# Kernel optimization log

Hardware: AMD Instinct MI355X
Metric: run time of the kernel (lower is better)

Reference implementation:

```python
import jax, jax.numpy as jnp
import numpy as np

B, Nc, Ns, Nz, Nx, K = 2, 128, 2048, 256, 256, 4


def setup_inputs() -> dict:
    key = jax.random.key(0)
    k1, k2, k3 = jax.random.split(key, 3)
    # RF channel data: [B, Nc, Ns, K]
    rf = jax.random.normal(k1, (B, Nc, Ns, K), dtype=jnp.float32)
    # Imaging grid point coordinates (meters), ~4 cm field: [B, Nz, Nx, 3]
    g = jax.random.uniform(k2, (B, Nz, Nx, 3), dtype=jnp.float32) * 0.04
    # Receiver element positions (meters): [B, Nc, 3]
    pr = jax.random.uniform(k3, (B, Nc, 3), dtype=jnp.float32) * 0.04
    # Acquisition params per batch: [c0 (m/s), fs (Hz), t0 (s), unused]
    p = jnp.tile(jnp.array([1540.0, 40.0e6, 0.0, 0.0], dtype=jnp.float32), (B, 1))
    return {"rf": rf, "g": g, "pr": pr, "p": p}


def reference(rf, g, pr, p):
    # rf: [B, Nc, Ns, K]; g: [B, Nz, Nx, 3]; pr: [B, Nc, 3]; p: [B, 4]
    b, nc, ns, k = rf.shape
    nz, nx = g.shape[1], g.shape[2]
    m = nz * nx

    c0 = p[:, 0][:, None, None, None]
    fs = p[:, 1][:, None, None, None]
    t0 = p[:, 2][:, None, None, None]

    d_tx = g[..., 2]  # [B, Nz, Nx] transmit path = depth coordinate
    # receive path: distance from each receiver to each pixel -> [B, Nc, Nz, Nx]
    d_rx = jnp.linalg.norm(g[:, None, :, :, :] - pr[:, :, None, None, :], axis=-1)
    # fractional sample index of the round-trip delay
    samples = fs * (t0 + (d_rx + d_tx[:, None, :, :])) / c0  # [B, Nc, Nz, Nx]
    s = samples.reshape(b, nc, m)

    # batch_interp_regular_1d_grid with x_ref_min=0, x_ref_max=Ns-1 on Ns points
    # -> unit grid spacing, constant extension (clamp) outside the grid.
    s = jnp.clip(s, 0.0, float(ns - 1))
    i0 = jnp.clip(jnp.floor(s).astype(jnp.int32), 0, ns - 2)  # [B, Nc, M]
    w = (s - i0.astype(s.dtype))[..., None]                   # [B, Nc, M, 1]

    idx0 = jnp.broadcast_to(i0[..., None], (b, nc, m, k))
    y0 = jnp.take_along_axis(rf, idx0, axis=2)      # [B, Nc, M, K]
    y1 = jnp.take_along_axis(rf, idx0 + 1, axis=2)  # [B, Nc, M, K]
    interp = y0 * (1.0 - w) + y1 * w

    # delay-and-sum over channels, then back to image layout [B, Nz, Nx, K]
    y_das = jnp.sum(interp, axis=1).reshape(b, nz, nx, k)
    return y_das
```

## Files before the change

### kernel.cpp

```cpp
#include <hip/hip_runtime.h>


#define NBATCH 2
#define NC 128
#define NS 2048
#define NK 4
#define NM 65536

#define THREADS 1024
#define PX_PER_THREAD 4
#define PX_PER_BLOCK (THREADS * PX_PER_THREAD)
#define C_PER_BLOCK 16
#define N_CHUNKS (NC / C_PER_BLOCK)
#define N_TILES (NM / PX_PER_BLOCK)
#define NBLOCKS (NBATCH * N_TILES * N_CHUNKS)
#define SLICE_F4 (NS * NK / 4)

#define PART_BYTES ((size_t)N_CHUNKS * NBATCH * NM * NK * 4)

typedef float f32x4 __attribute__((ext_vector_type(4)));

__device__ __forceinline__ void stage_channel(const float* slice, float4* lbuf, int t) {
#pragma unroll
    for (int r = 0; r < SLICE_F4 / THREADS; ++r) {
        const int d = r * THREADS + t;
        __builtin_amdgcn_global_load_lds(
            (const __attribute__((address_space(1))) void*)(slice + (size_t)d * 4),
            (__attribute__((address_space(3))) void*)(lbuf + d),
            16, 0, 0);
    }
}

template <bool ATOMIC>
__global__ __launch_bounds__(THREADS, 8) void das_kernel(
    const float* __restrict__ rf, const float* __restrict__ g,
    const float* __restrict__ pr, const float* __restrict__ p,
    float* __restrict__ dst)
{
    __shared__ float4 sbuf[2][SLICE_F4];

    const int bid   = blockIdx.x;
    const int chunk = bid & (N_CHUNKS - 1);
    const int tile  = (bid >> 3) & (N_TILES - 1);
    const int b     = bid >> 7;
    const int t     = threadIdx.x;
    const int px0   = tile * PX_PER_BLOCK;

    const float c0v = p[b * 4 + 0];
    const float fsv = p[b * 4 + 1];
    const float t0v = p[b * 4 + 2];
    const float scale = fsv / c0v;
    const float sb0   = scale * t0v;

    float gx[PX_PER_THREAD], gy[PX_PER_THREAD], gzv[PX_PER_THREAD];
#pragma unroll
    for (int j = 0; j < PX_PER_THREAD; ++j) {
        const int m = px0 + j * THREADS + t;
        const float* gp = g + ((size_t)b * NM + m) * 3;
        gx[j]  = gp[0];
        gy[j]  = gp[1];
        gzv[j] = gp[2];
    }

    float4 acc[PX_PER_THREAD];
#pragma unroll
    for (int j = 0; j < PX_PER_THREAD; ++j) acc[j] = make_float4(0.f, 0.f, 0.f, 0.f);

    const int ch0 = chunk * C_PER_BLOCK;
    const float* slice0 = rf + (size_t)(b * NC + ch0) * NS * NK;

    stage_channel(slice0, &sbuf[0][0], t);

    for (int cc = 0; cc < C_PER_BLOCK; ++cc) {
        __syncthreads();
        if (cc + 1 < C_PER_BLOCK)
            stage_channel(slice0 + (size_t)(cc + 1) * NS * NK,
                          &sbuf[(cc + 1) & 1][0], t);

        const float4* lb = &sbuf[cc & 1][0];
        const float* prp = pr + ((size_t)(b * NC + ch0 + cc)) * 3;
        const float prx = prp[0], pry = prp[1], prz = prp[2];

#pragma unroll
        for (int j = 0; j < PX_PER_THREAD; ++j) {
            const float dx = gx[j]  - prx;
            const float dy = gy[j]  - pry;
            const float dz = gzv[j] - prz;
            const float drx = __builtin_amdgcn_sqrtf(fmaf(dx, dx, fmaf(dy, dy, dz * dz)));
            float s = fmaf(scale, gzv[j] + drx, sb0);
            s = fminf(fmaxf(s, 0.0f), (float)(NS - 1));
            const float fi = fminf(floorf(s), (float)(NS - 2));
            const float w  = s - fi;
            const float wm = 1.0f - w;
            const int i0 = (int)fi;
            const float4 y0 = lb[i0];
            const float4 y1 = lb[i0 + 1];
            acc[j].x = fmaf(y0.x, wm, fmaf(y1.x, w, acc[j].x));
            acc[j].y = fmaf(y0.y, wm, fmaf(y1.y, w, acc[j].y));
            acc[j].z = fmaf(y0.z, wm, fmaf(y1.z, w, acc[j].z));
            acc[j].w = fmaf(y0.w, wm, fmaf(y1.w, w, acc[j].w));
        }
    }

    if (ATOMIC) {
        float* ob = dst + (size_t)b * NM * NK;
#pragma unroll
        for (int j = 0; j < PX_PER_THREAD; ++j) {
            const int m = px0 + j * THREADS + t;
            float* op = ob + (size_t)m * NK;
            atomicAdd(op + 0, acc[j].x);
            atomicAdd(op + 1, acc[j].y);
            atomicAdd(op + 2, acc[j].z);
            atomicAdd(op + 3, acc[j].w);
        }
    } else {
        f32x4* pw = (f32x4*)dst + (size_t)(chunk * NBATCH + b) * NM;
#pragma unroll
        for (int j = 0; j < PX_PER_THREAD; ++j) {
            const int m = px0 + j * THREADS + t;
            const f32x4 v = {acc[j].x, acc[j].y, acc[j].z, acc[j].w};
            __builtin_nontemporal_store(v, pw + m);
        }
    }
}

__global__ __launch_bounds__(256) void reduce_kernel(
    const f32x4* __restrict__ part, f32x4* __restrict__ out)
{
    const int i = blockIdx.x * 256 + threadIdx.x;
    const size_t stride = (size_t)NBATCH * NM;
    f32x4 a = __builtin_nontemporal_load(part + i);
#pragma unroll
    for (int c = 1; c < N_CHUNKS; ++c) {
        const f32x4 v = __builtin_nontemporal_load(part + c * stride + i);
        a += v;
    }
    out[i] = a;
}

extern "C" void kernel_launch(void* const* d_in, const int* in_sizes, int n_in,
                              void* d_out, int out_size, void* d_ws, size_t ws_size,
                              hipStream_t stream) {
    (void)in_sizes; (void)n_in;
    const float* rf = (const float*)d_in[0];
    const float* g  = (const float*)d_in[1];
    const float* pr = (const float*)d_in[2];
    const float* p  = (const float*)d_in[3];
    float* out = (float*)d_out;

    if (ws_size >= PART_BYTES) {
        das_kernel<false><<<NBLOCKS, THREADS, 0, stream>>>(rf, g, pr, p, (float*)d_ws);
        reduce_kernel<<<(NBATCH * NM) / 256, 256, 0, stream>>>((const f32x4*)d_ws,
                                                               (f32x4*)out);
    } else {
        (void)hipMemsetAsync(d_out, 0, (size_t)out_size * sizeof(float), stream);
        das_kernel<true><<<NBLOCKS, THREADS, 0, stream>>>(rf, g, pr, p, out);
    }
}
```

Baseline: 92.10 us.

## Stage RF slices in LDS as fp16 via register prefetch instead of direct global-to-LDS

Each channel's RF slice is now converted to half precision and stored in LDS at half the size. Staging goes through registers: the next slice is loaded early and written to LDS after the compute loop, replacing the asynchronous global_load_lds path. The aim is to halve LDS footprint and gather bandwidth. The costs are extra convert instructions on both store and gather, fp16 rounding of the RF data, and a halved occupancy hint in launch_bounds.

Result: faster. 86.97 us, median of 3 (-5.6%).

```diff
diff --git a/kernel.cpp b/kernel.cpp
--- a/kernel.cpp
+++ b/kernel.cpp
@@ -1,4 +1,5 @@
 #include <hip/hip_runtime.h>
+#include <hip/hip_fp16.h>
 
 
 #define NBATCH 2
@@ -14,30 +15,29 @@
 #define N_CHUNKS (NC / C_PER_BLOCK)
 #define N_TILES (NM / PX_PER_BLOCK)
 #define NBLOCKS (NBATCH * N_TILES * N_CHUNKS)
-#define SLICE_F4 (NS * NK / 4)
 
 #define PART_BYTES ((size_t)N_CHUNKS * NBATCH * NM * NK * 4)
 
 typedef float f32x4 __attribute__((ext_vector_type(4)));
 
-__device__ __forceinline__ void stage_channel(const float* slice, float4* lbuf, int t) {
-#pragma unroll
-    for (int r = 0; r < SLICE_F4 / THREADS; ++r) {
-        const int d = r * THREADS + t;
-        __builtin_amdgcn_global_load_lds(
-            (const __attribute__((address_space(1))) void*)(slice + (size_t)d * 4),
-            (__attribute__((address_space(3))) void*)(lbuf + d),
-            16, 0, 0);
-    }
+__device__ __forceinline__ uint4 cvt8(float4 a, float4 b) {
+    const __half2 h0 = __floats2half2_rn(a.x, a.y);
+    const __half2 h1 = __floats2half2_rn(a.z, a.w);
+    const __half2 h2 = __floats2half2_rn(b.x, b.y);
+    const __half2 h3 = __floats2half2_rn(b.z, b.w);
+    return make_uint4(__builtin_bit_cast(unsigned, h0),
+                      __builtin_bit_cast(unsigned, h1),
+                      __builtin_bit_cast(unsigned, h2),
+                      __builtin_bit_cast(unsigned, h3));
 }
 
 template <bool ATOMIC>
-__global__ __launch_bounds__(THREADS, 8) void das_kernel(
+__global__ __launch_bounds__(THREADS, 4) void das_kernel(
     const float* __restrict__ rf, const float* __restrict__ g,
     const float* __restrict__ pr, const float* __restrict__ p,
     float* __restrict__ dst)
 {
-    __shared__ float4 sbuf[2][SLICE_F4];
+    __shared__ uint4 sbuf[2][NS / 2];
 
     const int bid   = blockIdx.x;
     const int chunk = bid & (N_CHUNKS - 1);
@@ -69,15 +69,24 @@
     const int ch0 = chunk * C_PER_BLOCK;
     const float* slice0 = rf + (size_t)(b * NC + ch0) * NS * NK;
 
-    stage_channel(slice0, &sbuf[0][0], t);
+    {
+        const float4* s4 = (const float4*)slice0;
+        const float4 a0 = s4[2 * t];
+        const float4 a1 = s4[2 * t + 1];
+        sbuf[0][t] = cvt8(a0, a1);
+    }
 
     for (int cc = 0; cc < C_PER_BLOCK; ++cc) {
         __syncthreads();
-        if (cc + 1 < C_PER_BLOCK)
-            stage_channel(slice0 + (size_t)(cc + 1) * NS * NK,
-                          &sbuf[(cc + 1) & 1][0], t);
 
-        const float4* lb = &sbuf[cc & 1][0];
+        float4 a0, a1;
+        if (cc + 1 < C_PER_BLOCK) {
+            const float4* s4 = (const float4*)(slice0 + (size_t)(cc + 1) * NS * NK);
+            a0 = s4[2 * t];
+            a1 = s4[2 * t + 1];
+        }
+
+        const uint2* lb = (const uint2*)&sbuf[cc & 1][0];
         const float* prp = pr + ((size_t)(b * NC + ch0 + cc)) * 3;
         const float prx = prp[0], pry = prp[1], prz = prp[2];
 
@@ -93,13 +102,20 @@
             const float w  = s - fi;
             const float wm = 1.0f - w;
             const int i0 = (int)fi;
-            const float4 y0 = lb[i0];
-            const float4 y1 = lb[i0 + 1];
-            acc[j].x = fmaf(y0.x, wm, fmaf(y1.x, w, acc[j].x));
-            acc[j].y = fmaf(y0.y, wm, fmaf(y1.y, w, acc[j].y));
-            acc[j].z = fmaf(y0.z, wm, fmaf(y1.z, w, acc[j].z));
-            acc[j].w = fmaf(y0.w, wm, fmaf(y1.w, w, acc[j].w));
+            const uint2 u0 = lb[i0];
+            const uint2 u1 = lb[i0 + 1];
+            const float2 y0a = __half22float2(__builtin_bit_cast(__half2, u0.x));
+            const float2 y0b = __half22float2(__builtin_bit_cast(__half2, u0.y));
+            const float2 y1a = __half22float2(__builtin_bit_cast(__half2, u1.x));
+            const float2 y1b = __half22float2(__builtin_bit_cast(__half2, u1.y));
+            acc[j].x = fmaf(y0a.x, wm, fmaf(y1a.x, w, acc[j].x));
+            acc[j].y = fmaf(y0a.y, wm, fmaf(y1a.y, w, acc[j].y));
+            acc[j].z = fmaf(y0b.x, wm, fmaf(y1b.x, w, acc[j].z));
+            acc[j].w = fmaf(y0b.y, wm, fmaf(y1b.y, w, acc[j].w));
         }
+
+        if (cc + 1 < C_PER_BLOCK)
+            sbuf[(cc + 1) & 1][t] = cvt8(a0, a1);
     }
 
     if (ATOMIC) {
```
